# Kernel tuning notes

Measured on AMD Instinct MI355X. Metric: run time of the kernel, lower is better.

Reference implementation:

```python
import jax, jax.numpy as jnp
import numpy as np

N_CLUSTERS = 512
TEMPERATURE = 0.1


def setup_inputs() -> dict:
    key = jax.random.key(0)
    k1, k2 = jax.random.split(key)
    x = jax.random.normal(k1, (32, 1024, 256), dtype=jnp.float32)
    centroids = jax.random.normal(k2, (N_CLUSTERS, 256), dtype=jnp.float32)
    return {"x": x, "centroids": centroids}


def reference(x, centroids):
    # Flatten non-cluster axes into a sample axis: [N, D]
    B, S, D = x.shape
    xf = x.reshape(-1, D)  # [N, D]
    x_sq = jnp.sum(xf * xf, axis=-1, keepdims=True)           # [N, 1]
    c_sq = jnp.sum(centroids * centroids, axis=-1)             # [K]
    cross = jnp.einsum('nd,kd->nk', xf, centroids)             # [N, K]
    dists = x_sq - 2.0 * cross + c_sq[None, :]                 # [N, K]
    # Temperature-scaled soft assignments
    assignments = jax.nn.softmax(-dists / TEMPERATURE, axis=-1)  # [N, K]
    # Restore leading (non-feature) dims, append cluster axis
    return assignments.reshape(B, S, N_CLUSTERS)
```

## Files before the change

### kernel.cpp

```cpp
#include <hip/hip_runtime.h>

#define NROWS 32768
#define KC 512
#define DDIM 256
#define BM 32
#define BK 32
#define KCH (DDIM / BK)

typedef __attribute__((ext_vector_type(8))) short bf16x8;
typedef __attribute__((ext_vector_type(4))) float f32x4;

union U8 { unsigned short u[8]; bf16x8 v; };

__device__ __forceinline__ unsigned short f2bf(float f) {
    union { float f; unsigned int u; } a; a.f = f;
    unsigned int r = a.u + 0x7fffu + ((a.u >> 16) & 1u);
    return (unsigned short)(r >> 16);
}
__device__ __forceinline__ float bf2f(unsigned short h) {
    union { unsigned int u; float f; } a; a.u = ((unsigned int)h) << 16;
    return a.f;
}

__global__ __launch_bounds__(64) void prep_c(const float* __restrict__ c,
                                             unsigned short* __restrict__ bhi,
                                             unsigned short* __restrict__ blo,
                                             float* __restrict__ csq10) {
    const int n = blockIdx.x, lane = threadIdx.x;
    const int d0 = lane * 4;
    float4 v = ((const float4*)(c + (size_t)n * DDIM))[lane];
    float vv[4] = {v.x, v.y, v.z, v.w};
    unsigned short hh[4], ll[4];
    float ssq = 0.f;
    #pragma unroll
    for (int i = 0; i < 4; ++i) {
        ssq += vv[i] * vv[i];
        hh[i] = f2bf(vv[i]);
        ll[i] = f2bf(vv[i] - bf2f(hh[i]));
    }
    #pragma unroll
    for (int off = 32; off; off >>= 1) ssq += __shfl_xor(ssq, off);
    if (lane == 0) csq10[n] = 10.f * ssq;
    const int ks = d0 >> 5;
    const int q  = (d0 >> 3) & 3;
    const int t  = n >> 4, cc = n & 15;
    const size_t dst = ((size_t)(ks * 32 + t) * 64 + (q * 16 + cc)) * 8 + (d0 & 7);
    *(ushort4*)(bhi + dst) = make_ushort4(hh[0], hh[1], hh[2], hh[3]);
    *(ushort4*)(blo + dst) = make_ushort4(ll[0], ll[1], ll[2], ll[3]);
}

__global__ __launch_bounds__(256, 3) void kmeans_mfma(
    const float* __restrict__ x, const unsigned short* __restrict__ bhi,
    const unsigned short* __restrict__ blo, const float* __restrict__ csq10,
    float* __restrict__ out) {
    __shared__ __align__(16) float lbuf[16 * 516];
    __shared__ float red[2][4][BM];

    const int tid  = threadIdx.x;
    const int wn   = tid >> 6, lane = tid & 63;
    const int cc   = lane & 15, q = lane >> 4;
    const int row0 = blockIdx.x * BM;

    f32x4 acc[2][8];
    #pragma unroll
    for (int mt = 0; mt < 2; ++mt)
        #pragma unroll
        for (int t = 0; t < 8; ++t) acc[mt][t] = (f32x4){0.f, 0.f, 0.f, 0.f};

    const float* xA0 = x + (size_t)(row0 + cc) * DDIM + q * 8;
    const float* xA1 = xA0 + (size_t)16 * DDIM;

    const unsigned short* bhp = bhi + ((size_t)(wn * 8) << 9) + lane * 8;
    const unsigned short* blp = blo + ((size_t)(wn * 8) << 9) + lane * 8;
    bf16x8 pb[2][2][2];
    pb[0][0][0] = *(const bf16x8*)(bhp);
    pb[0][0][1] = *(const bf16x8*)(blp);
    pb[0][1][0] = *(const bf16x8*)(bhp + 512);
    pb[0][1][1] = *(const bf16x8*)(blp + 512);
    float4 c00 = *(const float4*)xA0;
    float4 c01 = *(const float4*)(xA0 + 4);
    float4 c10 = *(const float4*)xA1;
    float4 c11 = *(const float4*)(xA1 + 4);

    for (int ks = 0; ks < KCH; ++ks) {
        float4 n00, n01, n10, n11;
        if (ks < KCH - 1) {
            const int kn = (ks + 1) * BK;
            n00 = *(const float4*)(xA0 + kn);
            n01 = *(const float4*)(xA0 + kn + 4);
            n10 = *(const float4*)(xA1 + kn);
            n11 = *(const float4*)(xA1 + kn + 4);
        }
        bf16x8 ah[2], al[2];
        {
            float v0[8] = {c00.x, c00.y, c00.z, c00.w, c01.x, c01.y, c01.z, c01.w};
            float v1[8] = {c10.x, c10.y, c10.z, c10.w, c11.x, c11.y, c11.z, c11.w};
            U8 H0, L0, H1, L1;
            #pragma unroll
            for (int e = 0; e < 8; ++e) {
                H0.u[e] = f2bf(v0[e]); L0.u[e] = f2bf(v0[e] - bf2f(H0.u[e]));
                H1.u[e] = f2bf(v1[e]); L1.u[e] = f2bf(v1[e] - bf2f(H1.u[e]));
            }
            ah[0] = H0.v; al[0] = L0.v; ah[1] = H1.v; al[1] = L1.v;
        }
        #pragma unroll
        for (int tg = 0; tg < 4; ++tg) {
            const int par = tg & 1, nxt = par ^ 1;
            if (tg < 3) {
                pb[nxt][0][0] = *(const bf16x8*)(bhp + (2 * tg + 2) * 512);
                pb[nxt][0][1] = *(const bf16x8*)(blp + (2 * tg + 2) * 512);
                pb[nxt][1][0] = *(const bf16x8*)(bhp + (2 * tg + 3) * 512);
                pb[nxt][1][1] = *(const bf16x8*)(blp + (2 * tg + 3) * 512);
            } else if (ks < KCH - 1) {
                pb[nxt][0][0] = *(const bf16x8*)(bhp + 32 * 512);
                pb[nxt][0][1] = *(const bf16x8*)(blp + 32 * 512);
                pb[nxt][1][0] = *(const bf16x8*)(bhp + 33 * 512);
                pb[nxt][1][1] = *(const bf16x8*)(blp + 33 * 512);
            }
            #pragma unroll
            for (int p = 0; p < 3; ++p)
                #pragma unroll
                for (int tt = 0; tt < 2; ++tt) {
                    const int t = 2 * tg + tt;
                    const bf16x8 a0 = (p == 2) ? al[0] : ah[0];
                    const bf16x8 a1 = (p == 2) ? al[1] : ah[1];
                    const bf16x8 b  = (p == 1) ? pb[par][tt][1] : pb[par][tt][0];
                    acc[0][t] = __builtin_amdgcn_mfma_f32_16x16x32_bf16(a0, b, acc[0][t], 0, 0, 0);
                    acc[1][t] = __builtin_amdgcn_mfma_f32_16x16x32_bf16(a1, b, acc[1][t], 0, 0, 0);
                }
        }
        bhp += 32 * 512;
        blp += 32 * 512;
        c00 = n00; c01 = n01; c10 = n10; c11 = n11;
    }

    float csqv[8];
    #pragma unroll
    for (int t = 0; t < 8; ++t) csqv[t] = csq10[wn * 128 + t * 16 + cc];
    const int rb = q * 4;
    float M[2][4], I[2][4];
    #pragma unroll
    for (int mt = 0; mt < 2; ++mt)
        #pragma unroll
        for (int g = 0; g < 4; ++g) {
            float pm = -1e30f;
            #pragma unroll
            for (int t = 0; t < 8; ++t) pm = fmaxf(pm, 20.f * acc[mt][t][g] - csqv[t]);
            #pragma unroll
            for (int off = 1; off < 16; off <<= 1) pm = fmaxf(pm, __shfl_xor(pm, off));
            if (cc == 0) red[0][wn][rb + mt * 16 + g] = pm;
        }
    __syncthreads();
    #pragma unroll
    for (int mt = 0; mt < 2; ++mt)
        #pragma unroll
        for (int g = 0; g < 4; ++g) {
            const int ri = rb + mt * 16 + g;
            const float m = fmaxf(fmaxf(red[0][0][ri], red[0][1][ri]),
                                  fmaxf(red[0][2][ri], red[0][3][ri]));
            M[mt][g] = m;
            float ps = 0.f;
            #pragma unroll
            for (int t = 0; t < 8; ++t) ps += __expf(20.f * acc[mt][t][g] - csqv[t] - m);
            #pragma unroll
            for (int off = 1; off < 16; off <<= 1) ps += __shfl_xor(ps, off);
            if (cc == 0) red[1][wn][ri] = ps;
        }
    __syncthreads();
    #pragma unroll
    for (int mt = 0; mt < 2; ++mt)
        #pragma unroll
        for (int g = 0; g < 4; ++g) {
            const int ri = rb + mt * 16 + g;
            I[mt][g] = 1.f / (red[1][0][ri] + red[1][1][ri] +
                              red[1][2][ri] + red[1][3][ri]);
        }

    #pragma unroll
    for (int p = 0; p < 2; ++p) {
        const int mt = p;
        #pragma unroll
        for (int g = 0; g < 4; ++g) {
            const int   lr = q * 4 + g;
            const float mg = M[mt][g], ig = I[mt][g];
            #pragma unroll
            for (int t = 0; t < 8; ++t)
                lbuf[lr * 516 + wn * 128 + t * 16 + cc] =
                    __expf(20.f * acc[mt][t][g] - csqv[t] - mg) * ig;
        }
        __syncthreads();
        #pragma unroll
        for (int j = 0; j < 8; ++j) {
            const int f    = j * 256 + tid;
            const int lrow = f >> 7;
            const int c4   = f & 127;
            float4    v    = *(const float4*)&lbuf[lrow * 516 + c4 * 4];
            *(float4*)(out + (size_t)(row0 + p * 16 + lrow) * KC + c4 * 4) = v;
        }
        __syncthreads();
    }
}

extern "C" void kernel_launch(void* const* d_in, const int* in_sizes, int n_in,
                              void* d_out, int out_size, void* d_ws, size_t ws_size,
                              hipStream_t stream) {
    const float* x   = (const float*)d_in[0];
    const float* c   = (const float*)d_in[1];
    float*       out = (float*)d_out;

    unsigned short* bhi   = (unsigned short*)d_ws;
    unsigned short* blo   = bhi + (size_t)KCH * KC * BK;
    float*          csq10 = (float*)(blo + (size_t)KCH * KC * BK);

    prep_c<<<KC, 64, 0, stream>>>(c, bhi, blo, csq10);
    kmeans_mfma<<<NROWS / BM, 256, 0, stream>>>(x, bhi, blo, csq10, out);
}
```

Before: 143.1 us.

## Enlarge row tile to 64 with 8 waves each covering 64 centroids

Doubles the rows per block to 64 and uses 512 threads (8 waves), so each wave computes a 64x64 output tile instead of a 32x128 one. Each centroid B fragment loaded from global memory is now reused across four row tiles, which cuts per-block B-operand traffic relative to the MFMA work. The x operand is prefetched one K-chunk ahead and the B fragments are double-buffered across K-chunks, with the K loop fully unrolled. The cost is that the x hi/lo bf16 split is repeated in every wave for all 64 rows, softmax reductions span 8 waves, and the larger block plus launch bounds of 2 change occupancy and register pressure.

```diff
diff --git a/kernel.cpp b/kernel.cpp
--- a/kernel.cpp
+++ b/kernel.cpp
@@ -3,7 +3,7 @@
 #define NROWS 32768
 #define KC 512
 #define DDIM 256
-#define BM 32
+#define BM 64
 #define BK 32
 #define KCH (DDIM / BK)
 
@@ -49,149 +49,148 @@
     *(ushort4*)(blo + dst) = make_ushort4(ll[0], ll[1], ll[2], ll[3]);
 }
 
-__global__ __launch_bounds__(256, 3) void kmeans_mfma(
+__global__ __launch_bounds__(512, 2) void kmeans_mfma(
     const float* __restrict__ x, const unsigned short* __restrict__ bhi,
     const unsigned short* __restrict__ blo, const float* __restrict__ csq10,
     float* __restrict__ out) {
     __shared__ __align__(16) float lbuf[16 * 516];
-    __shared__ float red[2][4][BM];
+    __shared__ float red[2][8][BM];
 
     const int tid  = threadIdx.x;
     const int wn   = tid >> 6, lane = tid & 63;
     const int cc   = lane & 15, q = lane >> 4;
     const int row0 = blockIdx.x * BM;
 
-    f32x4 acc[2][8];
-    #pragma unroll
-    for (int mt = 0; mt < 2; ++mt)
-        #pragma unroll
-        for (int t = 0; t < 8; ++t) acc[mt][t] = (f32x4){0.f, 0.f, 0.f, 0.f};
+    f32x4 acc[4][4];
+    #pragma unroll
+    for (int mt = 0; mt < 4; ++mt)
+        #pragma unroll
+        for (int tt = 0; tt < 4; ++tt) acc[mt][tt] = (f32x4){0.f, 0.f, 0.f, 0.f};
 
     const float* xA0 = x + (size_t)(row0 + cc) * DDIM + q * 8;
-    const float* xA1 = xA0 + (size_t)16 * DDIM;
-
-    const unsigned short* bhp = bhi + ((size_t)(wn * 8) << 9) + lane * 8;
-    const unsigned short* blp = blo + ((size_t)(wn * 8) << 9) + lane * 8;
-    bf16x8 pb[2][2][2];
-    pb[0][0][0] = *(const bf16x8*)(bhp);
-    pb[0][0][1] = *(const bf16x8*)(blp);
-    pb[0][1][0] = *(const bf16x8*)(bhp + 512);
-    pb[0][1][1] = *(const bf16x8*)(blp + 512);
-    float4 c00 = *(const float4*)xA0;
-    float4 c01 = *(const float4*)(xA0 + 4);
-    float4 c10 = *(const float4*)xA1;
-    float4 c11 = *(const float4*)(xA1 + 4);
-
+    const unsigned short* bhp = bhi + ((size_t)(wn * 4) << 9) + lane * 8;
+    const unsigned short* blp = blo + ((size_t)(wn * 4) << 9) + lane * 8;
+
+    float4 ra[8];
+    bf16x8 pbh[2][4], pbl[2][4];
+
+    #pragma unroll
+    for (int mt = 0; mt < 4; ++mt) {
+        ra[2 * mt]     = *(const float4*)(xA0 + (size_t)mt * 16 * DDIM);
+        ra[2 * mt + 1] = *(const float4*)(xA0 + (size_t)mt * 16 * DDIM + 4);
+    }
+    #pragma unroll
+    for (int tt = 0; tt < 4; ++tt) {
+        pbh[0][tt] = *(const bf16x8*)(bhp + tt * 512);
+        pbl[0][tt] = *(const bf16x8*)(blp + tt * 512);
+    }
+
+    #pragma unroll
     for (int ks = 0; ks < KCH; ++ks) {
-        float4 n00, n01, n10, n11;
+        const int par = ks & 1, nxt = par ^ 1;
+        bf16x8 ah[4], al[4];
+        #pragma unroll
+        for (int mt = 0; mt < 4; ++mt) {
+            float v[8] = {ra[2 * mt].x, ra[2 * mt].y, ra[2 * mt].z, ra[2 * mt].w,
+                          ra[2 * mt + 1].x, ra[2 * mt + 1].y, ra[2 * mt + 1].z,
+                          ra[2 * mt + 1].w};
+            U8 H, L;
+            #pragma unroll
+            for (int e = 0; e < 8; ++e) {
+                H.u[e] = f2bf(v[e]);
+                L.u[e] = f2bf(v[e] - bf2f(H.u[e]));
+            }
+            ah[mt] = H.v; al[mt] = L.v;
+        }
         if (ks < KCH - 1) {
             const int kn = (ks + 1) * BK;
-            n00 = *(const float4*)(xA0 + kn);
-            n01 = *(const float4*)(xA0 + kn + 4);
-            n10 = *(const float4*)(xA1 + kn);
-            n11 = *(const float4*)(xA1 + kn + 4);
-        }
-        bf16x8 ah[2], al[2];
-        {
-            float v0[8] = {c00.x, c00.y, c00.z, c00.w, c01.x, c01.y, c01.z, c01.w};
-            float v1[8] = {c10.x, c10.y, c10.z, c10.w, c11.x, c11.y, c11.z, c11.w};
-            U8 H0, L0, H1, L1;
-            #pragma unroll
-            for (int e = 0; e < 8; ++e) {
-                H0.u[e] = f2bf(v0[e]); L0.u[e] = f2bf(v0[e] - bf2f(H0.u[e]));
-                H1.u[e] = f2bf(v1[e]); L1.u[e] = f2bf(v1[e] - bf2f(H1.u[e]));
-            }
-            ah[0] = H0.v; al[0] = L0.v; ah[1] = H1.v; al[1] = L1.v;
-        }
-        #pragma unroll
-        for (int tg = 0; tg < 4; ++tg) {
-            const int par = tg & 1, nxt = par ^ 1;
-            if (tg < 3) {
-                pb[nxt][0][0] = *(const bf16x8*)(bhp + (2 * tg + 2) * 512);
-                pb[nxt][0][1] = *(const bf16x8*)(blp + (2 * tg + 2) * 512);
-                pb[nxt][1][0] = *(const bf16x8*)(bhp + (2 * tg + 3) * 512);
-                pb[nxt][1][1] = *(const bf16x8*)(blp + (2 * tg + 3) * 512);
-            } else if (ks < KCH - 1) {
-                pb[nxt][0][0] = *(const bf16x8*)(bhp + 32 * 512);
-                pb[nxt][0][1] = *(const bf16x8*)(blp + 32 * 512);
-                pb[nxt][1][0] = *(const bf16x8*)(bhp + 33 * 512);
-                pb[nxt][1][1] = *(const bf16x8*)(blp + 33 * 512);
-            }
-            #pragma unroll
-            for (int p = 0; p < 3; ++p)
+            #pragma unroll
+            for (int mt = 0; mt < 4; ++mt) {
+                ra[2 * mt]     = *(const float4*)(xA0 + (size_t)mt * 16 * DDIM + kn);
+                ra[2 * mt + 1] = *(const float4*)(xA0 + (size_t)mt * 16 * DDIM + kn + 4);
+            }
+            #pragma unroll
+            for (int tt = 0; tt < 4; ++tt) {
+                pbh[nxt][tt] = *(const bf16x8*)(bhp + ((ks + 1) * 32 + tt) * 512);
+                pbl[nxt][tt] = *(const bf16x8*)(blp + ((ks + 1) * 32 + tt) * 512);
+            }
+        }
+        #pragma unroll
+        for (int p = 0; p < 3; ++p)
+            #pragma unroll
+            for (int tt = 0; tt < 4; ++tt) {
+                const bf16x8 b = (p == 1) ? pbl[par][tt] : pbh[par][tt];
                 #pragma unroll
-                for (int tt = 0; tt < 2; ++tt) {
-                    const int t = 2 * tg + tt;
-                    const bf16x8 a0 = (p == 2) ? al[0] : ah[0];
-                    const bf16x8 a1 = (p == 2) ? al[1] : ah[1];
-                    const bf16x8 b  = (p == 1) ? pb[par][tt][1] : pb[par][tt][0];
-                    acc[0][t] = __builtin_amdgcn_mfma_f32_16x16x32_bf16(a0, b, acc[0][t], 0, 0, 0);
-                    acc[1][t] = __builtin_amdgcn_mfma_f32_16x16x32_bf16(a1, b, acc[1][t], 0, 0, 0);
+                for (int mt = 0; mt < 4; ++mt) {
+                    const bf16x8 a = (p == 2) ? al[mt] : ah[mt];
+                    acc[mt][tt] = __builtin_amdgcn_mfma_f32_16x16x32_bf16(a, b, acc[mt][tt], 0, 0, 0);
                 }
-        }
-        bhp += 32 * 512;
-        blp += 32 * 512;
-        c00 = n00; c01 = n01; c10 = n10; c11 = n11;
-    }
-
-    float csqv[8];
-    #pragma unroll
-    for (int t = 0; t < 8; ++t) csqv[t] = csq10[wn * 128 + t * 16 + cc];
+            }
+    }
+
+    float csqv[4];
+    #pragma unroll
+    for (int tt = 0; tt < 4; ++tt) csqv[tt] = csq10[wn * 64 + tt * 16 + cc];
     const int rb = q * 4;
-    float M[2][4], I[2][4];
-    #pragma unroll
-    for (int mt = 0; mt < 2; ++mt)
+    float M[4][4], I[4][4];
+    #pragma unroll
+    for (int mt = 0; mt < 4; ++mt)
         #pragma unroll
         for (int g = 0; g < 4; ++g) {
             float pm = -1e30f;
             #pragma unroll
-            for (int t = 0; t < 8; ++t) pm = fmaxf(pm, 20.f * acc[mt][t][g] - csqv[t]);
+            for (int tt = 0; tt < 4; ++tt)
+                pm = fmaxf(pm, 20.f * acc[mt][tt][g] - csqv[tt]);
             #pragma unroll
             for (int off = 1; off < 16; off <<= 1) pm = fmaxf(pm, __shfl_xor(pm, off));
-            if (cc == 0) red[0][wn][rb + mt * 16 + g] = pm;
+            if (cc == 0) red[0][wn][mt * 16 + rb + g] = pm;
         }
     __syncthreads();
     #pragma unroll
-    for (int mt = 0; mt < 2; ++mt)
-        #pragma unroll
-        for (int g = 0; g < 4; ++g) {
-            const int ri = rb + mt * 16 + g;
-            const float m = fmaxf(fmaxf(red[0][0][ri], red[0][1][ri]),
-                                  fmaxf(red[0][2][ri], red[0][3][ri]));
+    for (int mt = 0; mt < 4; ++mt)
+        #pragma unroll
+        for (int g = 0; g < 4; ++g) {
+            const int ri = mt * 16 + rb + g;
+            float m = fmaxf(fmaxf(fmaxf(red[0][0][ri], red[0][1][ri]),
+                                  fmaxf(red[0][2][ri], red[0][3][ri])),
+                            fmaxf(fmaxf(red[0][4][ri], red[0][5][ri]),
+                                  fmaxf(red[0][6][ri], red[0][7][ri])));
             M[mt][g] = m;
             float ps = 0.f;
             #pragma unroll
-            for (int t = 0; t < 8; ++t) ps += __expf(20.f * acc[mt][t][g] - csqv[t] - m);
+            for (int tt = 0; tt < 4; ++tt)
+                ps += __expf(20.f * acc[mt][tt][g] - csqv[tt] - m);
             #pragma unroll
             for (int off = 1; off < 16; off <<= 1) ps += __shfl_xor(ps, off);
             if (cc == 0) red[1][wn][ri] = ps;
         }
     __syncthreads();
     #pragma unroll
-    for (int mt = 0; mt < 2; ++mt)
-        #pragma unroll
-        for (int g = 0; g < 4; ++g) {
-            const int ri = rb + mt * 16 + g;
-            I[mt][g] = 1.f / (red[1][0][ri] + red[1][1][ri] +
-                              red[1][2][ri] + red[1][3][ri]);
-        }
-
-    #pragma unroll
-    for (int p = 0; p < 2; ++p) {
-        const int mt = p;
-        #pragma unroll
-        for (int g = 0; g < 4; ++g) {
-            const int   lr = q * 4 + g;
-            const float mg = M[mt][g], ig = I[mt][g];
-            #pragma unroll
-            for (int t = 0; t < 8; ++t)
-                lbuf[lr * 516 + wn * 128 + t * 16 + cc] =
-                    __expf(20.f * acc[mt][t][g] - csqv[t] - mg) * ig;
+    for (int mt = 0; mt < 4; ++mt)
+        #pragma unroll
+        for (int g = 0; g < 4; ++g) {
+            const int ri = mt * 16 + rb + g;
+            I[mt][g] = 1.f / (((red[1][0][ri] + red[1][1][ri]) +
+                               (red[1][2][ri] + red[1][3][ri])) +
+                              ((red[1][4][ri] + red[1][5][ri]) +
+                               (red[1][6][ri] + red[1][7][ri])));
+        }
+
+    #pragma unroll
+    for (int p = 0; p < 4; ++p) {
+        #pragma unroll
+        for (int g = 0; g < 4; ++g) {
+            const int   lr = rb + g;
+            const float mg = M[p][g], ig = I[p][g];
+            #pragma unroll
+            for (int tt = 0; tt < 4; ++tt)
+                lbuf[lr * 516 + wn * 64 + tt * 16 + cc] =
+                    __expf(20.f * acc[p][tt][g] - csqv[tt] - mg) * ig;
         }
         __syncthreads();
         #pragma unroll
-        for (int j = 0; j < 8; ++j) {
-            const int f    = j * 256 + tid;
+        for (int j = 0; j < 4; ++j) {
+            const int f    = j * 512 + tid;
             const int lrow = f >> 7;
             const int c4   = f & 127;
             float4    v    = *(const float4*)&lbuf[lrow * 516 + c4 * 4];
@@ -213,5 +212,5 @@
     float*          csq10 = (float*)(blo + (size_t)KCH * KC * BK);
 
     prep_c<<<KC, 64, 0, stream>>>(c, bhi, blo, csq10);
-    kmeans_mfma<<<NROWS / BM, 256, 0, stream>>>(x, bhi, blo, csq10, out);
-}
+    kmeans_mfma<<<NROWS / BM, 512, 0, stream>>>(x, bhi, blo, csq10, out);
+}
```

Result: slower. 148.0 us (+3.4%).
